# Kernel tuning notes

Hardware: AMD Instinct MI355X
Metric: run time of the kernel (lower is better)

The kernel has to match this reference:

```python
import jax, jax.numpy as jnp
import numpy as np

NUM_HEADS = 16
Q_HEAD_DIM = 128
KV_HEAD_DIM = 128
ROPE_DIM = 64
LATENT_DIM = 512
INPUT_DIM = 2048


def setup_inputs() -> dict:
    key = jax.random.key(0)
    ks = jax.random.split(key, 7)
    B, S, D = 2, 2048, INPUT_DIM
    x = jax.random.normal(ks[0], (B, S, D), dtype=jnp.float32)
    positions = jnp.arange(S, dtype=jnp.int32)
    # weights stored as (in, out); torch Linear computes x @ W.T with W:(out,in)
    sc = lambda fan_in: 1.0 / np.sqrt(fan_in)
    Wq = jax.random.normal(ks[1], (D, NUM_HEADS * Q_HEAD_DIM), dtype=jnp.float32) * sc(D)
    Wc = jax.random.normal(ks[2], (D, LATENT_DIM), dtype=jnp.float32) * sc(D)
    Wk = jax.random.normal(ks[3], (LATENT_DIM, NUM_HEADS * KV_HEAD_DIM), dtype=jnp.float32) * sc(LATENT_DIM)
    Wv = jax.random.normal(ks[4], (LATENT_DIM, NUM_HEADS * KV_HEAD_DIM), dtype=jnp.float32) * sc(LATENT_DIM)
    Wo = jax.random.normal(ks[5], (NUM_HEADS * KV_HEAD_DIM, D), dtype=jnp.float32) * sc(NUM_HEADS * KV_HEAD_DIM)
    return {"x": x, "positions": positions, "Wq": Wq, "Wc": Wc, "Wk": Wk, "Wv": Wv, "Wo": Wo}


def _apply_rope_q(q, positions):
    # partial RoPE on first ROPE_DIM dims of q: (B,S,H,Dq)
    half = ROPE_DIM // 2
    inv_freq = 1.0 / (10000.0 ** (jnp.arange(0, ROPE_DIM, 2, dtype=jnp.float32) / ROPE_DIM))
    freqs = positions.astype(jnp.float32)[:, None] * inv_freq[None, :]  # (S, half)
    cos = jnp.cos(freqs)[None, :, None, :]  # (1,S,1,half)
    sin = jnp.sin(freqs)[None, :, None, :]
    x1 = q[..., :half]
    x2 = q[..., half:ROPE_DIM]
    rotated = jnp.concatenate([x1 * cos - x2 * sin, x1 * sin + x2 * cos], axis=-1)
    return jnp.concatenate([rotated, q[..., ROPE_DIM:]], axis=-1)


def reference(x, positions, Wq, Wc, Wk, Wv, Wo):
    B, S, _ = x.shape
    H, Dq, Dk = NUM_HEADS, Q_HEAD_DIM, KV_HEAD_DIM
    q = (x @ Wq).reshape(B, S, H, Dq)
    kv_latent = x @ Wc                       # (B,S,latent) low-rank compression
    k = (kv_latent @ Wk).reshape(B, S, H, Dk)
    v = (kv_latent @ Wv).reshape(B, S, H, Dk)
    q = _apply_rope_q(q, positions)          # RoPE applied to q only (as in source)
    scale = 1.0 / jnp.sqrt(jnp.float32(Dq))
    scores = jnp.einsum("bqhd,bkhd->bhqk", q, k) * scale
    attn = jax.nn.softmax(scores, axis=-1)
    out = jnp.einsum("bhqk,bkhd->bqhd", attn, v).reshape(B, S, H * Dk)
    return out @ Wo
```

## Files before the change

kernel.cpp:

```cpp
#include <hip/hip_runtime.h>
#include <math.h>


typedef __attribute__((ext_vector_type(8))) short bf16x8;
typedef __attribute__((ext_vector_type(4))) float f32x4;
typedef __attribute__((ext_vector_type(16))) float f32x16;

#define GLDS(gp, lp)                                                         \
  __builtin_amdgcn_global_load_lds(                                          \
      (const __attribute__((address_space(1))) void*)(gp),                   \
      (__attribute__((address_space(3))) void*)(lp), 16, 0, 0)

__device__ __forceinline__ short f2bf(float f) {
  unsigned u = __builtin_bit_cast(unsigned, f);
  u += 0x7fffu + ((u >> 16) & 1u);
  return (short)(u >> 16);
}
__device__ __forceinline__ float b2f(short x) {
  unsigned u = ((unsigned)(unsigned short)x) << 16;
  return __builtin_bit_cast(float, u);
}
__device__ __forceinline__ unsigned cvtpk(float lo, float hi) {
  unsigned r;
  asm("v_cvt_pk_bf16_f32 %0, %1, %2" : "=v"(r) : "v"(lo), "v"(hi));
  return r;
}

__device__ __forceinline__ void transpose_body(const float* __restrict__ W,
                                               short* __restrict__ Wt,
                                               int K, int N, int n0, int k0,
                                               float (*tile)[33]) {
  int tx = threadIdx.x & 31, ty = threadIdx.x >> 5;
#pragma unroll
  for (int i = 0; i < 4; ++i)
    tile[ty + i * 8][tx] = W[(size_t)(k0 + ty + i * 8) * N + n0 + tx];
  __syncthreads();
#pragma unroll
  for (int i = 0; i < 4; ++i)
    Wt[(size_t)(n0 + ty + i * 8) * K + k0 + tx] = f2bf(tile[tx][ty + i * 8]);
}

__global__ void prep_kernel(const float* __restrict__ x, short* __restrict__ xb,
                            const float* __restrict__ Wq, short* __restrict__ wqT,
                            const float* __restrict__ Wo, short* __restrict__ woT,
                            const float* __restrict__ Wc, short* __restrict__ wcT,
                            const float* __restrict__ Wk, short* __restrict__ wkT,
                            const float* __restrict__ Wv, short* __restrict__ wvT,
                            const int* __restrict__ pos, float* __restrict__ cosT,
                            float* __restrict__ sinT) {
  __shared__ float tile[32][33];
  const int bid = blockIdx.x;
  if (bid < 8192) {
    int i = bid * 256 + threadIdx.x;
    float4 v = ((const float4*)x)[i];
    ushort4 o;
    o.x = (unsigned short)f2bf(v.x);
    o.y = (unsigned short)f2bf(v.y);
    o.z = (unsigned short)f2bf(v.z);
    o.w = (unsigned short)f2bf(v.w);
    ((ushort4*)xb)[i] = o;
  } else if (bid < 16384) {
    int local = bid - 8192;
    int z = local >> 12, rem = local & 4095;
    transpose_body(z ? Wo : Wq, z ? woT : wqT, 2048, 2048,
                   (rem & 63) * 32, (rem >> 6) * 32, tile);
  } else if (bid < 17408) {
    int local = bid - 16384;
    transpose_body(Wc, wcT, 2048, 512, (local & 15) * 32, (local >> 4) * 32, tile);
  } else if (bid < 19456) {
    int local = bid - 17408;
    int z = local >> 10, rem = local & 1023;
    transpose_body(z ? Wv : Wk, z ? wvT : wkT, 512, 2048,
                   (rem & 63) * 32, (rem >> 6) * 32, tile);
  } else {
    int idx = (bid - 19456) * 256 + threadIdx.x;
    int s = idx >> 5, i = idx & 31;
    float p = (float)pos[s];
    float freq = p * powf(10000.0f, -(float)(2 * i) / 64.0f);
    float sv, cv;
    sincosf(freq, &sv, &cv);
    cosT[idx] = cv;
    sinT[idx] = sv;
  }
}

template <int MODE>
__device__ __forceinline__ void gemm_core(const short* __restrict__ A,
                                          const short* __restrict__ Bt,
                                          void* __restrict__ Cv,
                                          int N, int K, int bm, int bn,
                                          short* sm) {
  const int tid  = threadIdx.x;
  const int lane = tid & 63;
  const int w    = tid >> 6;
  const int col  = lane & 15, g = lane >> 4;
  const int wr = w >> 1, wc = w & 1;

  f32x4 zero4 = {0.f, 0.f, 0.f, 0.f};
  f32x4 acc[4][4];
#pragma unroll
  for (int m = 0; m < 4; ++m)
#pragma unroll
    for (int n = 0; n < 4; ++n) acc[m][n] = zero4;

  const int sr = tid >> 3;
  const int sk = tid & 7;

  auto STAGE = [&](int buf, int t) {
#pragma unroll
    for (int i = 0; i < 4; ++i) {
      int r = i * 32 + sr;
      int c = (sk ^ (r & 7)) << 3;
      GLDS(A  + (size_t)(bm + r) * K + t * 64 + c,
           sm + buf * 8192 + i * 2048 + w * 512);
      GLDS(Bt + (size_t)(bn + r) * K + t * 64 + c,
           sm + 16384 + buf * 8192 + i * 2048 + w * 512);
    }
  };

  const int nt = K >> 6;
  STAGE(0, 0);
  __syncthreads();
  int buf = 0;
  for (int t = 0; t < nt; ++t) {
    if (t + 1 < nt) STAGE(buf ^ 1, t + 1);
    const short* As = sm + buf * 8192;
    const short* Bs = sm + 16384 + buf * 8192;
#pragma unroll
    for (int kk = 0; kk < 2; ++kk) {
      bf16x8 la[4], lb[4];
#pragma unroll
      for (int m = 0; m < 4; ++m) {
        int row = wr * 64 + m * 16 + col;
        la[m] = *(const bf16x8*)(As + row * 64 + (((kk * 4 + g) ^ (row & 7)) << 3));
      }
#pragma unroll
      for (int n = 0; n < 4; ++n) {
        int row = wc * 64 + n * 16 + col;
        lb[n] = *(const bf16x8*)(Bs + row * 64 + (((kk * 4 + g) ^ (row & 7)) << 3));
      }
#pragma unroll
      for (int m = 0; m < 4; ++m)
#pragma unroll
        for (int n = 0; n < 4; ++n)
          acc[m][n] = __builtin_amdgcn_mfma_f32_16x16x32_bf16(la[m], lb[n], acc[m][n], 0, 0, 0);
    }
    __syncthreads();
    buf ^= 1;
  }

  const int orow0 = bm + wr * 64;
  const int ocol0 = bn + wc * 64;
  if (MODE == 0) {
    short* C = (short*)Cv;
#pragma unroll
    for (int m = 0; m < 4; ++m)
#pragma unroll
      for (int n = 0; n < 4; ++n)
#pragma unroll
        for (int r = 0; r < 4; ++r)
          C[(size_t)(orow0 + m * 16 + g * 4 + r) * N + ocol0 + n * 16 + col] =
              f2bf(acc[m][n][r]);
  } else if (MODE == 1) {
    float* C = (float*)Cv;
#pragma unroll
    for (int m = 0; m < 4; ++m)
#pragma unroll
      for (int n = 0; n < 4; ++n)
#pragma unroll
        for (int r = 0; r < 4; ++r)
          C[(size_t)(orow0 + m * 16 + g * 4 + r) * N + ocol0 + n * 16 + col] =
              acc[m][n][r];
  } else {
    short* C = (short*)Cv;
#pragma unroll
    for (int m = 0; m < 4; ++m)
#pragma unroll
      for (int n = 0; n < 4; ++n) {
        int grow = orow0 + m * 16 + g * 4;
        int bb = grow >> 11, s = grow & 2047;
        int cn = ocol0 + n * 16 + col;
        ushort4 pk;
        pk.x = (unsigned short)f2bf(acc[m][n][0]);
        pk.y = (unsigned short)f2bf(acc[m][n][1]);
        pk.z = (unsigned short)f2bf(acc[m][n][2]);
        pk.w = (unsigned short)f2bf(acc[m][n][3]);
        *(ushort4*)(C + ((size_t)(bb * 2048 + cn)) * 2048 + s) = pk;
      }
  }
}

__global__ __launch_bounds__(256, 2) void gemm_qc(const short* __restrict__ xb,
                                                  const short* __restrict__ wqT,
                                                  const short* __restrict__ wcT,
                                                  short* __restrict__ qb,
                                                  short* __restrict__ kvb) {
  __shared__ alignas(16) short sm[32768];
  int x = blockIdx.x, y = blockIdx.y;
  if (x < 16) gemm_core<0>(xb, wqT, qb, 2048, 2048, y * 128, x * 128, sm);
  else        gemm_core<0>(xb, wcT, kvb, 512, 2048, y * 128, (x - 16) * 128, sm);
}
__global__ __launch_bounds__(256, 2) void gemm_kv(const short* __restrict__ kvb,
                                                  const short* __restrict__ wkT,
                                                  const short* __restrict__ wvT,
                                                  short* __restrict__ kb,
                                                  short* __restrict__ vtb) {
  __shared__ alignas(16) short sm[32768];
  int x = blockIdx.x, y = blockIdx.y;
  if (x < 16) gemm_core<0>(kvb, wkT, kb, 2048, 512, y * 128, x * 128, sm);
  else        gemm_core<2>(kvb, wvT, vtb, 2048, 512, y * 128, (x - 16) * 128, sm);
}
__global__ __launch_bounds__(256, 2) void gemm_wo(const short* __restrict__ obuf,
                                                  const short* __restrict__ woT,
                                                  float* __restrict__ out) {
  __shared__ alignas(16) short sm[32768];
  gemm_core<1>(obuf, woT, out, 2048, 2048, blockIdx.y * 128, blockIdx.x * 128, sm);
}

__global__ __launch_bounds__(256, 2) void attn_kernel(
    const short* __restrict__ qb, const short* __restrict__ kb,
    const short* __restrict__ vt, short* __restrict__ ob,
    const float* __restrict__ cosT, const float* __restrict__ sinT) {
  __shared__ alignas(16) short sm[32768];
  const int lane = threadIdx.x & 63, w = threadIdx.x >> 6;
  const int ql = lane & 31, hi = lane >> 5;
  const int qt = blockIdx.x >> 5, bh = blockIdx.x & 31;
  const int b = bh >> 4, h = bh & 15;
  const int q0w = qt * 128 + w * 32;
  const int qrow = q0w + ql;

  bf16x8 qf[8];
  {
    const short* qp = qb + ((size_t)(b * 2048 + qrow)) * 2048 + h * 128;
#pragma unroll
    for (int db = 0; db < 8; ++db) qf[db] = *(const bf16x8*)(qp + db * 16 + hi * 8);
    const float* cp = cosT + qrow * 32;
    const float* sp = sinT + qrow * 32;
#pragma unroll
    for (int db = 0; db < 2; ++db)
#pragma unroll
      for (int j = 0; j < 8; ++j) {
        int i = db * 16 + hi * 8 + j;
        float x1 = b2f(qf[db][j]), x2 = b2f(qf[db + 2][j]);
        float cv = cp[i], sv = sp[i];
        qf[db][j]     = f2bf(x1 * cv - x2 * sv);
        qf[db + 2][j] = f2bf(x1 * sv + x2 * cv);
      }
  }

  f32x16 o[4];
#pragma unroll
  for (int m4 = 0; m4 < 4; ++m4)
#pragma unroll
    for (int r = 0; r < 16; ++r) o[m4][r] = 0.f;
  float mrun = -3.0e38f, lrun = 0.f;

  auto STAGE = [&](int buf, int kt) {
#pragma unroll
    for (int i = 0; i < 4; ++i) {
      int r = w * 16 + i * 4 + (lane >> 4);
      int cch = lane & 15;
      const short* gp = kb + ((size_t)(b * 2048 + kt * 64 + r)) * 2048 + h * 128 +
                        ((cch ^ (r & 7)) << 3);
      GLDS(gp, sm + buf * 8192 + w * 2048 + i * 512);
    }
#pragma unroll
    for (int i = 0; i < 4; ++i) {
      int rd = w * 32 + i * 8 + (lane >> 3);
      int cch = lane & 7;
      const short* gp = vt + ((size_t)(b * 2048 + h * 128 + rd)) * 2048 + kt * 64 +
                        ((cch ^ (rd & 7)) << 3);
      GLDS(gp, sm + 16384 + buf * 8192 + w * 2048 + i * 512);
    }
  };

  const float cl2 = 0.12752744590518352f;
  STAGE(0, 0);
  __syncthreads();
  int buf = 0;
  for (int kt = 0; kt < 32; ++kt) {
    if (kt + 1 < 32) STAGE(buf ^ 1, kt + 1);
    const short* Ks = sm + buf * 8192;
    const short* Vs = sm + 16384 + buf * 8192;

    f32x16 skt[2];
    __builtin_amdgcn_s_setprio(1);
#pragma unroll
    for (int kb2 = 0; kb2 < 2; ++kb2) {
      f32x16 a0, a1;
#pragma unroll
      for (int r = 0; r < 16; ++r) { a0[r] = 0.f; a1[r] = 0.f; }
      int krow = kb2 * 32 + ql;
#pragma unroll
      for (int db = 0; db < 4; ++db) {
        bf16x8 kf = *(const bf16x8*)(Ks + krow * 128 + (((db * 2 + hi) ^ (krow & 7)) << 3));
        a0 = __builtin_amdgcn_mfma_f32_32x32x16_bf16(kf, qf[db], a0, 0, 0, 0);
      }
#pragma unroll
      for (int db = 4; db < 8; ++db) {
        bf16x8 kf = *(const bf16x8*)(Ks + krow * 128 + (((db * 2 + hi) ^ (krow & 7)) << 3));
        a1 = __builtin_amdgcn_mfma_f32_32x32x16_bf16(kf, qf[db], a1, 0, 0, 0);
      }
#pragma unroll
      for (int r = 0; r < 16; ++r) skt[kb2][r] = (a0[r] + a1[r]) * cl2;
    }
    __builtin_amdgcn_s_setprio(0);

    float t0, t1, t2, t3;
    t0 = fmaxf(fmaxf(fmaxf(fmaxf(skt[0][0], skt[0][4]), skt[0][8]),
                     fmaxf(skt[0][12], skt[1][0])),
               fmaxf(fmaxf(skt[1][4], skt[1][8]), skt[1][12]));
    t1 = fmaxf(fmaxf(fmaxf(fmaxf(skt[0][1], skt[0][5]), skt[0][9]),
                     fmaxf(skt[0][13], skt[1][1])),
               fmaxf(fmaxf(skt[1][5], skt[1][9]), skt[1][13]));
    t2 = fmaxf(fmaxf(fmaxf(fmaxf(skt[0][2], skt[0][6]), skt[0][10]),
                     fmaxf(skt[0][14], skt[1][2])),
               fmaxf(fmaxf(skt[1][6], skt[1][10]), skt[1][14]));
    t3 = fmaxf(fmaxf(fmaxf(fmaxf(skt[0][3], skt[0][7]), skt[0][11]),
                     fmaxf(skt[0][15], skt[1][3])),
               fmaxf(fmaxf(skt[1][7], skt[1][11]), skt[1][15]));
    float tmax = fmaxf(fmaxf(t0, t1), fmaxf(t2, t3));
    tmax = fmaxf(tmax, __shfl_xor(tmax, 32));

    if (!__all(tmax <= mrun + 8.0f)) {
      float mn = fmaxf(mrun, tmax);
      float fr = __builtin_amdgcn_exp2f(mrun - mn);
      mrun = mn;
      lrun *= fr;
#pragma unroll
      for (int m4 = 0; m4 < 4; ++m4)
#pragma unroll
        for (int r = 0; r < 16; ++r) o[m4][r] *= fr;
    }
    float s0 = 0.f, s1 = 0.f, s2 = 0.f, s3 = 0.f;
#pragma unroll
    for (int kb2 = 0; kb2 < 2; ++kb2)
#pragma unroll
      for (int r = 0; r < 16; r += 4) {
        skt[kb2][r]     = __builtin_amdgcn_exp2f(skt[kb2][r] - mrun);
        skt[kb2][r + 1] = __builtin_amdgcn_exp2f(skt[kb2][r + 1] - mrun);
        skt[kb2][r + 2] = __builtin_amdgcn_exp2f(skt[kb2][r + 2] - mrun);
        skt[kb2][r + 3] = __builtin_amdgcn_exp2f(skt[kb2][r + 3] - mrun);
        s0 += skt[kb2][r];     s1 += skt[kb2][r + 1];
        s2 += skt[kb2][r + 2]; s3 += skt[kb2][r + 3];
      }
    float psum = (s0 + s1) + (s2 + s3);
    psum += __shfl_xor(psum, 32);
    lrun += psum;

    bf16x8 pf[4];
#pragma unroll
    for (int kb2 = 0; kb2 < 2; ++kb2) {
#pragma unroll
      for (int half = 0; half < 2; ++half) {
        unsigned a0 = cvtpk(skt[kb2][half * 8 + 0], skt[kb2][half * 8 + 1]);
        unsigned a1 = cvtpk(skt[kb2][half * 8 + 2], skt[kb2][half * 8 + 3]);
        unsigned b0 = cvtpk(skt[kb2][half * 8 + 4], skt[kb2][half * 8 + 5]);
        unsigned b1 = cvtpk(skt[kb2][half * 8 + 6], skt[kb2][half * 8 + 7]);
        unsigned pa0 = __shfl_xor(a0, 32), pa1 = __shfl_xor(a1, 32);
        unsigned pb0 = __shfl_xor(b0, 32), pb1 = __shfl_xor(b1, 32);
        union { unsigned u[4]; bf16x8 v; } tmp;
        tmp.u[0] = hi ? pb0 : a0;
        tmp.u[1] = hi ? pb1 : a1;
        tmp.u[2] = hi ? b0 : pa0;
        tmp.u[3] = hi ? b1 : pa1;
        pf[kb2 * 2 + half] = tmp.v;
      }
    }

    __builtin_amdgcn_s_setprio(1);
#pragma unroll
    for (int m4 = 0; m4 < 4; ++m4) {
      int rd = m4 * 32 + ql;
#pragma unroll
      for (int ks = 0; ks < 4; ++ks) {
        bf16x8 vf = *(const bf16x8*)(Vs + rd * 64 + (((ks * 2 + hi) ^ (rd & 7)) << 3));
        o[m4] = __builtin_amdgcn_mfma_f32_32x32x16_bf16(vf, pf[ks], o[m4], 0, 0, 0);
      }
    }
    __builtin_amdgcn_s_setprio(0);
    __syncthreads();
    buf ^= 1;
  }

  float il = 1.0f / lrun;
  short* E = sm + w * 4352;
#pragma unroll
  for (int m4 = 0; m4 < 4; ++m4)
#pragma unroll
    for (int r = 0; r < 16; r += 2) {
      int d = m4 * 32 + (r & 3) + 8 * (r >> 2) + 4 * hi;
      unsigned pk = cvtpk(o[m4][r] * il, o[m4][r + 1] * il);
      *(unsigned*)(E + ql * 136 + d) = pk;
    }
  asm volatile("s_waitcnt lgkmcnt(0)" ::: "memory");
#pragma unroll
  for (int it = 0; it < 8; ++it) {
    int row = it * 4 + (lane >> 4);
    int ch = lane & 15;
    bf16x8 v = *(const bf16x8*)(E + row * 136 + ch * 8);
    *(bf16x8*)(ob + ((size_t)(b * 2048 + q0w + row)) * 2048 + h * 128 + ch * 8) = v;
  }
}

extern "C" void kernel_launch(void* const* d_in, const int* in_sizes, int n_in,
                              void* d_out, int out_size, void* d_ws, size_t ws_size,
                              hipStream_t stream) {
  (void)in_sizes; (void)n_in; (void)out_size; (void)ws_size;
  const float* x  = (const float*)d_in[0];
  const int*   pos = (const int*)d_in[1];
  const float* Wq = (const float*)d_in[2];
  const float* Wc = (const float*)d_in[3];
  const float* Wk = (const float*)d_in[4];
  const float* Wv = (const float*)d_in[5];
  const float* Wo = (const float*)d_in[6];

  char* ws = (char*)d_ws;
  short* xb   = (short*)(ws);
  short* qb   = (short*)(ws + 16777216);
  short* kvb  = (short*)(ws + 33554432);
  short* kb   = (short*)(ws + 37748736);
  short* vtb  = (short*)(ws + 54525952);
  short* obuf = (short*)(ws + 71303168);
  short* wqT  = (short*)(ws + 88080384);
  short* wcT  = (short*)(ws + 96468992);
  short* wkT  = (short*)(ws + 98566144);
  short* wvT  = (short*)(ws + 100663296);
  short* woT  = (short*)(ws + 102760448);
  float* cosT = (float*)(ws + 111149056);
  float* sinT = (float*)(ws + 111411200);

  prep_kernel<<<19712, 256, 0, stream>>>(x, xb, Wq, wqT, Wo, woT, Wc, wcT,
                                         Wk, wkT, Wv, wvT, pos, cosT, sinT);

  gemm_qc<<<dim3(20, 32), 256, 0, stream>>>(xb, wqT, wcT, qb, kvb);
  gemm_kv<<<dim3(32, 32), 256, 0, stream>>>(kvb, wkT, wvT, kb, vtb);

  attn_kernel<<<512, 256, 0, stream>>>(qb, kb, vtb, obuf, cosT, sinT);

  gemm_wo<<<dim3(16, 32), 256, 0, stream>>>(obuf, woT, (float*)d_out);
}
```

Baseline: 223.5 us.

## Swizzle GEMM block order per XCD, prescale Q, split PV accumulators

The three GEMM launches now use a 1D grid remapped so that consecutive blocks on the same XCD (block id mod 8) take neighbouring tiles, aiming for better L2 reuse. The attention kernel folds the softmax scale times log2(e) into Q once, after RoPE, instead of scaling every score tile. It also splits the PV MFMA chain into two independent accumulators so the dependent MFMAs can overlap, at the cost of 64 more accumulator registers. The RoPE frequency uses exp2f instead of powf. Scaling Q before the bf16 rounding changes the rounding slightly, and the extra registers may reduce occupancy or cause spills under launch_bounds(256,2).

```diff
diff --git a/kernel.cpp b/kernel.cpp
--- a/kernel.cpp
+++ b/kernel.cpp
@@ -76,7 +76,7 @@
     int idx = (bid - 19456) * 256 + threadIdx.x;
     int s = idx >> 5, i = idx & 31;
     float p = (float)pos[s];
-    float freq = p * powf(10000.0f, -(float)(2 * i) / 64.0f);
+    float freq = p * exp2f(-(float)i * 0.41524101186092029f);
     float sv, cv;
     sincosf(freq, &sv, &cv);
     cosT[idx] = cv;
@@ -196,7 +196,9 @@
                                                   short* __restrict__ qb,
                                                   short* __restrict__ kvb) {
   __shared__ alignas(16) short sm[32768];
-  int x = blockIdx.x, y = blockIdx.y;
+  int lin = blockIdx.x;
+  int swz = (lin & 7) * 80 + (lin >> 3);
+  int x = swz % 20, y = swz / 20;
   if (x < 16) gemm_core<0>(xb, wqT, qb, 2048, 2048, y * 128, x * 128, sm);
   else        gemm_core<0>(xb, wcT, kvb, 512, 2048, y * 128, (x - 16) * 128, sm);
 }
@@ -206,7 +208,9 @@
                                                   short* __restrict__ kb,
                                                   short* __restrict__ vtb) {
   __shared__ alignas(16) short sm[32768];
-  int x = blockIdx.x, y = blockIdx.y;
+  int lin = blockIdx.x;
+  int swz = (lin & 7) * 128 + (lin >> 3);
+  int x = swz & 31, y = swz >> 5;
   if (x < 16) gemm_core<0>(kvb, wkT, kb, 2048, 512, y * 128, x * 128, sm);
   else        gemm_core<2>(kvb, wvT, vtb, 2048, 512, y * 128, (x - 16) * 128, sm);
 }
@@ -214,7 +218,10 @@
                                                   const short* __restrict__ woT,
                                                   float* __restrict__ out) {
   __shared__ alignas(16) short sm[32768];
-  gemm_core<1>(obuf, woT, out, 2048, 2048, blockIdx.y * 128, blockIdx.x * 128, sm);
+  int lin = blockIdx.x;
+  int swz = (lin & 7) * 64 + (lin >> 3);
+  int x = swz & 15, y = swz >> 4;
+  gemm_core<1>(obuf, woT, out, 2048, 2048, y * 128, x * 128, sm);
 }
 
 __global__ __launch_bounds__(256, 2) void attn_kernel(
@@ -229,6 +236,8 @@
   const int q0w = qt * 128 + w * 32;
   const int qrow = q0w + ql;
 
+  const float cl2 = 0.12752744590518352f;
+
   bf16x8 qf[8];
   {
     const short* qp = qb + ((size_t)(b * 2048 + qrow)) * 2048 + h * 128;
@@ -243,16 +252,20 @@
         int i = db * 16 + hi * 8 + j;
         float x1 = b2f(qf[db][j]), x2 = b2f(qf[db + 2][j]);
         float cv = cp[i], sv = sp[i];
-        qf[db][j]     = f2bf(x1 * cv - x2 * sv);
-        qf[db + 2][j] = f2bf(x1 * sv + x2 * cv);
-      }
-  }
-
-  f32x16 o[4];
+        qf[db][j]     = f2bf((x1 * cv - x2 * sv) * cl2);
+        qf[db + 2][j] = f2bf((x1 * sv + x2 * cv) * cl2);
+      }
+#pragma unroll
+    for (int db = 4; db < 8; ++db)
+#pragma unroll
+      for (int j = 0; j < 8; ++j) qf[db][j] = f2bf(b2f(qf[db][j]) * cl2);
+  }
+
+  f32x16 o[4], o2[4];
 #pragma unroll
   for (int m4 = 0; m4 < 4; ++m4)
 #pragma unroll
-    for (int r = 0; r < 16; ++r) o[m4][r] = 0.f;
+    for (int r = 0; r < 16; ++r) { o[m4][r] = 0.f; o2[m4][r] = 0.f; }
   float mrun = -3.0e38f, lrun = 0.f;
 
   auto STAGE = [&](int buf, int kt) {
@@ -274,7 +287,6 @@
     }
   };
 
-  const float cl2 = 0.12752744590518352f;
   STAGE(0, 0);
   __syncthreads();
   int buf = 0;
@@ -302,7 +314,7 @@
         a1 = __builtin_amdgcn_mfma_f32_32x32x16_bf16(kf, qf[db], a1, 0, 0, 0);
       }
 #pragma unroll
-      for (int r = 0; r < 16; ++r) skt[kb2][r] = (a0[r] + a1[r]) * cl2;
+      for (int r = 0; r < 16; ++r) skt[kb2][r] = a0[r] + a1[r];
     }
     __builtin_amdgcn_s_setprio(0);
 
@@ -330,7 +342,7 @@
 #pragma unroll
       for (int m4 = 0; m4 < 4; ++m4)
 #pragma unroll
-        for (int r = 0; r < 16; ++r) o[m4][r] *= fr;
+        for (int r = 0; r < 16; ++r) { o[m4][r] *= fr; o2[m4][r] *= fr; }
     }
     float s0 = 0.f, s1 = 0.f, s2 = 0.f, s3 = 0.f;
 #pragma unroll
@@ -373,9 +385,14 @@
     for (int m4 = 0; m4 < 4; ++m4) {
       int rd = m4 * 32 + ql;
 #pragma unroll
-      for (int ks = 0; ks < 4; ++ks) {
+      for (int ks = 0; ks < 2; ++ks) {
         bf16x8 vf = *(const bf16x8*)(Vs + rd * 64 + (((ks * 2 + hi) ^ (rd & 7)) << 3));
         o[m4] = __builtin_amdgcn_mfma_f32_32x32x16_bf16(vf, pf[ks], o[m4], 0, 0, 0);
+      }
+#pragma unroll
+      for (int ks = 2; ks < 4; ++ks) {
+        bf16x8 vf = *(const bf16x8*)(Vs + rd * 64 + (((ks * 2 + hi) ^ (rd & 7)) << 3));
+        o2[m4] = __builtin_amdgcn_mfma_f32_32x32x16_bf16(vf, pf[ks], o2[m4], 0, 0, 0);
       }
     }
     __builtin_amdgcn_s_setprio(0);
@@ -390,7 +407,8 @@
 #pragma unroll
     for (int r = 0; r < 16; r += 2) {
       int d = m4 * 32 + (r & 3) + 8 * (r >> 2) + 4 * hi;
-      unsigned pk = cvtpk(o[m4][r] * il, o[m4][r + 1] * il);
+      unsigned pk = cvtpk((o[m4][r] + o2[m4][r]) * il,
+                          (o[m4][r + 1] + o2[m4][r + 1]) * il);
       *(unsigned*)(E + ql * 136 + d) = pk;
     }
   asm volatile("s_waitcnt lgkmcnt(0)" ::: "memory");
@@ -433,10 +451,10 @@
   prep_kernel<<<19712, 256, 0, stream>>>(x, xb, Wq, wqT, Wo, woT, Wc, wcT,
                                          Wk, wkT, Wv, wvT, pos, cosT, sinT);
 
-  gemm_qc<<<dim3(20, 32), 256, 0, stream>>>(xb, wqT, wcT, qb, kvb);
-  gemm_kv<<<dim3(32, 32), 256, 0, stream>>>(kvb, wkT, wvT, kb, vtb);
+  gemm_qc<<<640, 256, 0, stream>>>(xb, wqT, wcT, qb, kvb);
+  gemm_kv<<<1024, 256, 0, stream>>>(kvb, wkT, wvT, kb, vtb);
 
   attn_kernel<<<512, 256, 0, stream>>>(qb, kb, vtb, obuf, cosT, sinT);
 
-  gemm_wo<<<dim3(16, 32), 256, 0, stream>>>(obuf, woT, (float*)d_out);
-}
+  gemm_wo<<<512, 256, 0, stream>>>(obuf, woT, (float*)d_out);
+}
```

New measurement: 228.5 us. 2.3% more time.
